# Performance work log

Hardware: AMD Instinct MI355X
Metric: run time of the kernel (lower is better)

Reference implementation:

```python
import jax, jax.numpy as jnp
import numpy as np

NUM_HEADS = 12   # H
NUM_TASKS = 4    # T
TOP_K = 2        # capacity_factor


def setup_inputs() -> dict:
    key = jax.random.key(0)
    ks = jax.random.split(key, 4)
    B, N, C = 2, 4100, 768  # N = NUM_TASKS + M, M = 4096
    x = jax.random.normal(ks[0], (B, N, C), dtype=jnp.float32)
    # torch.nn.Linear weights are [out_features, in_features]; y = x @ W.T
    qs_w = jax.random.normal(ks[1], (NUM_TASKS, C, C), dtype=jnp.float32) * 0.02
    kv_w = jax.random.normal(ks[2], (2 * C, C), dtype=jnp.float32) * 0.02
    experts_w = jax.random.normal(ks[3], (NUM_TASKS, C, C), dtype=jnp.float32) * 0.02
    return {"x": x, "qs_w": qs_w, "kv_w": kv_w, "experts_w": experts_w}


def reference(x, qs_w, kv_w, experts_w):
    B, N, C = x.shape
    T, H, K = NUM_TASKS, NUM_HEADS, TOP_K
    d = C // H
    M = N - T
    scale = d ** -0.5

    feature = x[:, T:, :]                                    # [B,M,C]
    kv = (feature @ kv_w.T).reshape(B, M, 2, H, d)
    k = jnp.transpose(kv[:, :, 0], (0, 2, 1, 3))             # [B,H,M,d]
    v = jnp.transpose(kv[:, :, 1], (0, 2, 1, 3))             # [B,H,M,d]

    # per-task q projections on task tokens (qs_w[t] is [out,in])
    q = jnp.einsum('btc,toc->bto', x[:, :T], qs_w)           # [B,T,C]
    q = q.reshape(B, T, H, d).transpose(0, 2, 1, 3)          # [B,H,T,d]

    attn = jnp.einsum('bhtd,bhmd->bhtm', q, k) * scale       # [B,H,T,M]
    topv, topi = jax.lax.top_k(attn, K)                      # [B,H,T,K]
    topw = jax.nn.softmax(topv, axis=-1)                     # softmax over top-k only

    # scatter softmaxed top-k back into dense [B,H,T,M] (indices unique per row)
    oh = jax.nn.one_hot(topi, M, dtype=x.dtype)              # [B,H,T,K,M]
    attn_topk = jnp.einsum('bhtk,bhtkm->bhtm', topw, oh)
    attn_token = jnp.einsum('bhtm,bhmd->bhtd', attn_topk, v)
    attn_token = attn_token.transpose(0, 2, 1, 3).reshape(B, T, C)   # [B,T,C]

    # gather top-k feature rows per head/task, weight, and scatter back
    fm = feature.reshape(B, M, H, d).transpose(0, 2, 1, 3)   # [B,H,M,d]
    feat_topk = jnp.take_along_axis(fm[:, :, None], topi[..., None], axis=3)  # [B,H,T,K,d]
    feat_topk = feat_topk * topw[..., None]
    # scatter to [B,H,T,M,d], then permute(0,2,3,1,4)+reshape -> [B,T,M,C]
    feat_pad = jnp.einsum('bhtkd,bhtkm->btmhd', feat_topk, oh).reshape(B, T, M, C)

    # per-task experts (no bias); einsum('btnc,btnc->bnc') with ones = sum over t
    feature_output = jnp.einsum('btmc,toc->bmo', feat_pad, experts_w)  # [B,M,C]
    token_output = jnp.einsum('btc,toc->bto', attn_token, experts_w)   # [B,T,C]

    return jnp.concatenate([token_output, feature_output], axis=1)     # [B,N,C]
```

## Files before the change

kernel.cpp:

```cpp
#include <hip/hip_runtime.h>
#include <math.h>

#define B_ 2
#define N_ 4100
#define C_ 768
#define T_ 4
#define H_ 12
#define D_ 64
#define M_ 4096
#define S_ 48
#define KS_ 6
#define KC_ 128
#define SEG_ 8
#define GRID_ 768
#define SCALE 0.125f

__device__ __forceinline__ bool better(float va, int ia, float vb, int ib) {
  return (va > vb) || (va == vb && ia < ib);
}

__device__ __forceinline__ void merge2(float& v1, int& i1, float& v2, int& i2,
                                       float ov1, int oi1, float ov2, int oi2) {
  if (better(ov1, oi1, v1, i1)) {
    float tv; int ti;
    tv = v1; ti = i1; v1 = ov1; i1 = oi1; ov1 = tv; oi1 = ti;
    tv = v2; ti = i2; v2 = ov2; i2 = oi2; ov2 = tv; oi2 = ti;
  }
  if (better(ov1, oi1, v2, i2)) { v2 = ov1; i2 = oi1; }
}

__global__ __launch_bounds__(256) void qkzero_kernel(const float* __restrict__ x,
    const float* __restrict__ qs_w, const float* __restrict__ kv_w,
    float* __restrict__ qk, float* __restrict__ out) {
  const int blk = blockIdx.x;
  const int tid = threadIdx.x;
  if (blk < B_ * S_) {
    const int h = blk % H_;
    const int t = (blk / H_) % T_;
    const int b = blk / S_;
    __shared__ float xs[C_];
    __shared__ float red[256];
    __shared__ float qseg[D_];
    for (int i = tid; i < C_; i += 256) xs[i] = x[((size_t)b * N_ + t) * C_ + i];
    __syncthreads();
    {
      const int j = tid & 63;
      const int pt = tid >> 6;
      const float* wr = qs_w + ((size_t)t * C_ + h * D_ + j) * C_ + pt * 192;
      float a = 0.f;
      for (int c = 0; c < 192; ++c) a += xs[pt * 192 + c] * wr[c];
      red[tid] = a;
    }
    __syncthreads();
    if (tid < 64)
      qseg[tid] = (red[tid] + red[tid + 64] + red[tid + 128] + red[tid + 192]) * SCALE;
    __syncthreads();
    for (int c = tid; c < C_; c += 256) {
      float a = 0.f;
      #pragma unroll 8
      for (int j = 0; j < 64; ++j) a += qseg[j] * kv_w[((size_t)(h * D_ + j)) * C_ + c];
      qk[(size_t)blk * C_ + c] = a;
    }
  } else {
    const int zb = blk - B_ * S_;
    const int NV4 = (B_ * N_ * C_) / 4;
    float4 z = make_float4(0.f, 0.f, 0.f, 0.f);
    float4* ov = (float4*)out;
    for (int i = zb * 256 + tid; i < NV4; i += (GRID_ - B_ * S_) * 256) ov[i] = z;
  }
}

__global__ __launch_bounds__(256) void score_kernel(const float* __restrict__ x,
    const float* __restrict__ qk, float* __restrict__ part) {
  const int mt = blockIdx.x & 63;
  const int b = blockIdx.x >> 6;
  const int kc = blockIdx.y;
  const int tid = threadIdx.x;
  const int m0 = mt * 64;

  __shared__ __align__(16) float fbuf[64][68];
  __shared__ __align__(16) float qkbuf[48][68];

  const int mg = tid & 15;
  const int sg = tid >> 4;

  float acc[4][3];
  #pragma unroll
  for (int u = 0; u < 4; ++u)
    #pragma unroll
    for (int i = 0; i < 3; ++i) acc[u][i] = 0.f;

  const float* xb = x + ((size_t)b * N_ + T_ + m0) * C_ + kc * KC_;
  const float* qkb = qk + (size_t)b * S_ * C_ + kc * KC_;

  for (int cc = 0; cc < KC_ / 64; ++cc) {
    __syncthreads();
    for (int i = tid; i < 64 * 16; i += 256) {
      int row = i >> 4, c4 = i & 15;
      *(float4*)&fbuf[row][c4 * 4] =
          *(const float4*)(xb + (size_t)row * C_ + cc * 64 + c4 * 4);
    }
    for (int i = tid; i < 48 * 16; i += 256) {
      int s = i >> 4, c4 = i & 15;
      *(float4*)&qkbuf[s][c4 * 4] =
          *(const float4*)(qkb + (size_t)s * C_ + cc * 64 + c4 * 4);
    }
    __syncthreads();
    #pragma unroll 4
    for (int c4 = 0; c4 < 16; ++c4) {
      float4 f[4], q[3];
      f[0] = *(const float4*)&fbuf[mg][c4 * 4];
      f[1] = *(const float4*)&fbuf[mg + 16][c4 * 4];
      f[2] = *(const float4*)&fbuf[mg + 32][c4 * 4];
      f[3] = *(const float4*)&fbuf[mg + 48][c4 * 4];
      q[0] = *(const float4*)&qkbuf[sg * 3 + 0][c4 * 4];
      q[1] = *(const float4*)&qkbuf[sg * 3 + 1][c4 * 4];
      q[2] = *(const float4*)&qkbuf[sg * 3 + 2][c4 * 4];
      #pragma unroll
      for (int u = 0; u < 4; ++u)
        #pragma unroll
        for (int i = 0; i < 3; ++i)
          acc[u][i] += f[u].x * q[i].x + f[u].y * q[i].y +
                       f[u].z * q[i].z + f[u].w * q[i].w;
    }
  }

  #pragma unroll
  for (int i = 0; i < 3; ++i) {
    int s = sg * 3 + i;
    float* pp = part + (((size_t)kc * B_ + b) * S_ + s) * M_ + m0 + mg;
    #pragma unroll
    for (int u = 0; u < 4; ++u) pp[16 * u] = acc[u][i];
  }
}

__global__ __launch_bounds__(256) void reduce_kernel(const float* __restrict__ part,
                                                     float* __restrict__ cand) {
  const int seg = blockIdx.x & 7;
  const int bs = blockIdx.x >> 3;
  const int tid = threadIdx.x;
  const size_t kstride = (size_t)B_ * S_ * M_;
  const float* p0 = part + (size_t)bs * M_ + seg * 512 + tid * 2;
  float a0 = 0.f, a1 = 0.f;
  #pragma unroll
  for (int kc = 0; kc < KS_; ++kc) {
    float2 v = *(const float2*)(p0 + kc * kstride);
    a0 += v.x; a1 += v.y;
  }
  const int mA = seg * 512 + tid * 2;
  float v1, v2; int i1, i2;
  if (better(a0, mA, a1, mA + 1)) { v1 = a0; i1 = mA; v2 = a1; i2 = mA + 1; }
  else                            { v1 = a1; i1 = mA + 1; v2 = a0; i2 = mA; }
  #pragma unroll
  for (int off = 1; off < 64; off <<= 1) {
    float ov1 = __shfl_xor(v1, off);
    int   oi1 = __shfl_xor(i1, off);
    float ov2 = __shfl_xor(v2, off);
    int   oi2 = __shfl_xor(i2, off);
    merge2(v1, i1, v2, i2, ov1, oi1, ov2, oi2);
  }
  __shared__ float cbuf[4][4];
  const int w = tid >> 6, lane = tid & 63;
  if (lane == 0) {
    cbuf[w][0] = v1; ((int*)cbuf[w])[1] = i1;
    cbuf[w][2] = v2; ((int*)cbuf[w])[3] = i2;
  }
  __syncthreads();
  if (tid == 0) {
    for (int ww = 1; ww < 4; ++ww)
      merge2(v1, i1, v2, i2, cbuf[ww][0], ((int*)cbuf[ww])[1],
             cbuf[ww][2], ((int*)cbuf[ww])[3]);
    ((float4*)cand)[blockIdx.x] =
        make_float4(v1, __int_as_float(i1), v2, __int_as_float(i2));
  }
}

__global__ __launch_bounds__(256) void gather_kernel(const float* __restrict__ x,
    const float* __restrict__ kv_w, const float* __restrict__ experts_w,
    const float* __restrict__ cand, float* __restrict__ out) {
  const int h = blockIdx.x % H_;
  const int t = (blockIdx.x / H_) % T_;
  const int b = blockIdx.x / S_;
  const int tid = threadIdx.x;

  __shared__ float f0[C_], f1[C_], fc[C_], red[256];
  __shared__ float attnh[D_];
  __shared__ float sel[4];

  if (tid < 8) {
    float4 cv = ((const float4*)cand)[blockIdx.x * 8 + tid];
    float v1 = cv.x, v2 = cv.z;
    int i1 = __float_as_int(cv.y), i2 = __float_as_int(cv.w);
    #pragma unroll
    for (int off = 1; off < 8; off <<= 1) {
      float ov1 = __shfl_xor(v1, off);
      int   oi1 = __shfl_xor(i1, off);
      float ov2 = __shfl_xor(v2, off);
      int   oi2 = __shfl_xor(i2, off);
      merge2(v1, i1, v2, i2, ov1, oi1, ov2, oi2);
    }
    if (tid == 0) {
      float w1 = 1.f / (1.f + expf(v2 - v1));
      ((int*)sel)[0] = i1; ((int*)sel)[1] = i2;
      sel[2] = w1; sel[3] = 1.f - w1;
    }
  }
  __syncthreads();
  const int i1 = ((const int*)sel)[0];
  const int i2 = ((const int*)sel)[1];
  const float w1 = sel[2], w2 = sel[3];

  const float* r0 = x + ((size_t)b * N_ + T_ + i1) * C_;
  const float* r1 = x + ((size_t)b * N_ + T_ + i2) * C_;
  for (int i = tid; i < C_; i += 256) {
    float a = r0[i], bb = r1[i];
    f0[i] = a; f1[i] = bb; fc[i] = w1 * a + w2 * bb;
  }
  __syncthreads();

  const int j = tid & 63, pt = tid >> 6;
  {
    const float* kr = kv_w + ((size_t)(C_ + h * D_ + j)) * C_ + pt * 192;
    float a = 0.f;
    for (int c = 0; c < 192; ++c) a += fc[pt * 192 + c] * kr[c];
    red[tid] = a;
  }
  __syncthreads();
  if (tid < 64)
    attnh[tid] = red[tid] + red[tid + 64] + red[tid + 128] + red[tid + 192];
  __syncthreads();

  const size_t ot = ((size_t)b * N_ + t) * C_;
  const size_t o0 = ((size_t)b * N_ + T_ + i1) * C_;
  const size_t o1 = ((size_t)b * N_ + T_ + i2) * C_;
  for (int o = tid; o < C_; o += 256) {
    const float* er = experts_w + ((size_t)t * C_ + o) * C_ + h * D_;
    float at = 0.f, a0 = 0.f, a1 = 0.f;
    #pragma unroll 8
    for (int c = 0; c < D_; ++c) {
      float e = er[c];
      at += e * attnh[c];
      a0 += e * f0[h * D_ + c];
      a1 += e * f1[h * D_ + c];
    }
    atomicAdd(&out[ot + o], at);
    atomicAdd(&out[o0 + o], w1 * a0);
    atomicAdd(&out[o1 + o], w2 * a1);
  }
}

extern "C" void kernel_launch(void* const* d_in, const int* in_sizes, int n_in,
                              void* d_out, int out_size, void* d_ws, size_t ws_size,
                              hipStream_t stream) {
  const float* x         = (const float*)d_in[0];
  const float* qs_w      = (const float*)d_in[1];
  const float* kv_w      = (const float*)d_in[2];
  const float* experts_w = (const float*)d_in[3];
  float* out = (float*)d_out;

  float* ws   = (float*)d_ws;
  float* qk   = ws;
  float* part = qk + (size_t)B_ * S_ * C_;
  float* cand = part + (size_t)KS_ * B_ * S_ * M_;

  hipLaunchKernelGGL(qkzero_kernel, dim3(GRID_),          dim3(256), 0, stream, x, qs_w, kv_w, qk, out);
  hipLaunchKernelGGL(score_kernel,  dim3(B_ * 64, KS_),   dim3(256), 0, stream, x, qk, part);
  hipLaunchKernelGGL(reduce_kernel, dim3(B_ * S_ * SEG_), dim3(256), 0, stream, part, cand);
  hipLaunchKernelGGL(gather_kernel, dim3(B_ * S_),        dim3(256), 0, stream, x, kv_w, experts_w, cand, out);
}
```

Measured before the change: 146.5 us.

## Restructure score kernel: stage only x in LDS, read interleaved qk from global

The score kernel now loads a 128-row by 96-column tile of features into shared memory once, then has each thread compute 24 scores for one feature row. The qk vectors are read straight from global memory in a new interleaved layout written by qkzero_kernel, so all lanes of a wavefront read the same address. This drops the per-chunk staging of qk and the double loop of syncs. In exchange the grid changes (8 k-splits of 96, 64 blocks per split), which enlarges the partial buffer, and each thread holds more accumulator registers.

```diff
diff --git a/kernel.cpp b/kernel.cpp
--- a/kernel.cpp
+++ b/kernel.cpp
@@ -9,8 +9,10 @@
 #define D_ 64
 #define M_ 4096
 #define S_ 48
-#define KS_ 6
-#define KC_ 128
+#define KS_ 8
+#define KC_ 96
+#define NJ_ 24
+#define MT2_ 128
 #define SEG_ 8
 #define GRID_ 768
 #define SCALE 0.125f
@@ -38,6 +40,7 @@
     const int h = blk % H_;
     const int t = (blk / H_) % T_;
     const int b = blk / S_;
+    const int s = t * H_ + h;
     __shared__ float xs[C_];
     __shared__ float red[256];
     __shared__ float qseg[D_];
@@ -59,7 +62,9 @@
       float a = 0.f;
       #pragma unroll 8
       for (int j = 0; j < 64; ++j) a += qseg[j] * kv_w[((size_t)(h * D_ + j)) * C_ + c];
-      qk[(size_t)blk * C_ + c] = a;
+      const int kc = c / KC_;
+      const int cr = c - kc * KC_;
+      qk[(((size_t)b * KS_ + kc) * NJ_ + (cr >> 2)) * (S_ * 4) + s * 4 + (cr & 3)] = a;
     }
   } else {
     const int zb = blk - B_ * S_;
@@ -72,65 +77,57 @@
 
 __global__ __launch_bounds__(256) void score_kernel(const float* __restrict__ x,
     const float* __restrict__ qk, float* __restrict__ part) {
-  const int mt = blockIdx.x & 63;
-  const int b = blockIdx.x >> 6;
+  const int bm = blockIdx.x & 31;
+  const int b = blockIdx.x >> 5;
   const int kc = blockIdx.y;
   const int tid = threadIdx.x;
-  const int m0 = mt * 64;
-
-  __shared__ __align__(16) float fbuf[64][68];
-  __shared__ __align__(16) float qkbuf[48][68];
-
-  const int mg = tid & 15;
-  const int sg = tid >> 4;
-
-  float acc[4][3];
-  #pragma unroll
-  for (int u = 0; u < 4; ++u)
+
+  __shared__ __align__(16) float fbuf[MT2_][100];
+
+  {
+    const char* xb = (const char*)(x + ((size_t)b * N_ + T_ + bm * MT2_) * C_ + kc * KC_);
     #pragma unroll
-    for (int i = 0; i < 3; ++i) acc[u][i] = 0.f;
-
-  const float* xb = x + ((size_t)b * N_ + T_ + m0) * C_ + kc * KC_;
-  const float* qkb = qk + (size_t)b * S_ * C_ + kc * KC_;
-
-  for (int cc = 0; cc < KC_ / 64; ++cc) {
-    __syncthreads();
-    for (int i = tid; i < 64 * 16; i += 256) {
-      int row = i >> 4, c4 = i & 15;
-      *(float4*)&fbuf[row][c4 * 4] =
-          *(const float4*)(xb + (size_t)row * C_ + cc * 64 + c4 * 4);
-    }
-    for (int i = tid; i < 48 * 16; i += 256) {
-      int s = i >> 4, c4 = i & 15;
-      *(float4*)&qkbuf[s][c4 * 4] =
-          *(const float4*)(qkb + (size_t)s * C_ + cc * 64 + c4 * 4);
-    }
-    __syncthreads();
-    #pragma unroll 4
-    for (int c4 = 0; c4 < 16; ++c4) {
-      float4 f[4], q[3];
-      f[0] = *(const float4*)&fbuf[mg][c4 * 4];
-      f[1] = *(const float4*)&fbuf[mg + 16][c4 * 4];
-      f[2] = *(const float4*)&fbuf[mg + 32][c4 * 4];
-      f[3] = *(const float4*)&fbuf[mg + 48][c4 * 4];
-      q[0] = *(const float4*)&qkbuf[sg * 3 + 0][c4 * 4];
-      q[1] = *(const float4*)&qkbuf[sg * 3 + 1][c4 * 4];
-      q[2] = *(const float4*)&qkbuf[sg * 3 + 2][c4 * 4];
+    for (int i = 0; i < 12; ++i) {
+      int g = i * 256 + tid;
+      int r = g / NJ_;
+      int j = g - r * NJ_;
+      float4 v = *(const float4*)(xb + (size_t)r * (C_ * 4) + j * 16);
+      *(float4*)&fbuf[r][j * 4] = v;
+    }
+  }
+  __syncthreads();
+
+  const int w = tid >> 6;
+  const int lane = tid & 63;
+  const int rr = (w & 1) * 64 + lane;
+  const int s0 = (w >> 1) * 24;
+
+  float acc[24];
+  #pragma unroll
+  for (int i = 0; i < 24; ++i) acc[i] = 0.f;
+
+  const float* qp = qk + (((size_t)b * KS_ + kc) * NJ_) * (S_ * 4) + s0 * 4;
+
+  for (int j = 0; j < NJ_; ++j) {
+    float4 f = *(const float4*)&fbuf[rr][j * 4];
+    const float* q = qp + j * (S_ * 4);
+    #pragma unroll
+    for (int sc = 0; sc < 24; sc += 8) {
+      float4 qv[8];
       #pragma unroll
-      for (int u = 0; u < 4; ++u)
-        #pragma unroll
-        for (int i = 0; i < 3; ++i)
-          acc[u][i] += f[u].x * q[i].x + f[u].y * q[i].y +
-                       f[u].z * q[i].z + f[u].w * q[i].w;
-    }
-  }
-
-  #pragma unroll
-  for (int i = 0; i < 3; ++i) {
-    int s = sg * 3 + i;
-    float* pp = part + (((size_t)kc * B_ + b) * S_ + s) * M_ + m0 + mg;
-    #pragma unroll
-    for (int u = 0; u < 4; ++u) pp[16 * u] = acc[u][i];
+      for (int si = 0; si < 8; ++si) qv[si] = *(const float4*)&q[(sc + si) * 4];
+      #pragma unroll
+      for (int si = 0; si < 8; ++si)
+        acc[sc + si] += f.x * qv[si].x + f.y * qv[si].y +
+                        f.z * qv[si].z + f.w * qv[si].w;
+    }
+  }
+
+  const int m = bm * MT2_ + rr;
+  #pragma unroll
+  for (int si = 0; si < 24; ++si) {
+    int s = s0 + si;
+    part[(((size_t)kc * B_ + b) * S_ + s) * M_ + m] = acc[si];
   }
 }
 
@@ -264,7 +261,7 @@
   float* cand = part + (size_t)KS_ * B_ * S_ * M_;
 
   hipLaunchKernelGGL(qkzero_kernel, dim3(GRID_),          dim3(256), 0, stream, x, qs_w, kv_w, qk, out);
-  hipLaunchKernelGGL(score_kernel,  dim3(B_ * 64, KS_),   dim3(256), 0, stream, x, qk, part);
+  hipLaunchKernelGGL(score_kernel,  dim3(B_ * 32, KS_),   dim3(256), 0, stream, x, qk, part);
   hipLaunchKernelGGL(reduce_kernel, dim3(B_ * S_ * SEG_), dim3(256), 0, stream, part, cand);
   hipLaunchKernelGGL(gather_kernel, dim3(B_ * S_),        dim3(256), 0, stream, x, kv_w, experts_w, cand, out);
 }
```

Measured after the change: 164.1 us. 1.12x slower.
